# Optimization experiments

Measured on AMD Instinct MI355X. Metric: run time of the kernel, lower is better.

The kernel has to match this reference:

```python
import jax, jax.numpy as jnp
import numpy as np

NUM_USERS = 100000
NUM_ITEMS = 200000
IN_DIM = 128
HID = 256
E = 500000


def setup_inputs() -> dict:
    key = jax.random.key(0)
    ks = jax.random.split(key, 12)
    s1 = 1.0 / np.sqrt(2 * IN_DIM)
    s2 = 1.0 / np.sqrt(HID)
    return {
        "user_embed": jax.random.normal(ks[0], (NUM_USERS, IN_DIM), jnp.float32),
        "item_embed": jax.random.normal(ks[1], (NUM_ITEMS, IN_DIM), jnp.float32),
        "u_clicks": jax.random.randint(ks[2], (E,), 0, NUM_USERS, jnp.int32),
        "v_clicks": jax.random.randint(ks[3], (E,), 0, NUM_ITEMS, jnp.int32),
        "u_buys": jax.random.randint(ks[4], (E,), 0, NUM_USERS, jnp.int32),
        "v_buys": jax.random.randint(ks[5], (E,), 0, NUM_ITEMS, jnp.int32),
        "W1_clicks": jax.random.normal(ks[6], (2 * IN_DIM, HID), jnp.float32) * s1,
        "b1_clicks": jnp.zeros((HID,), jnp.float32),
        "W2_clicks": jax.random.normal(ks[7], (HID,), jnp.float32) * s2,
        "b2_clicks": jnp.zeros((1,), jnp.float32),
        "W1_buys": jax.random.normal(ks[8], (2 * IN_DIM, HID), jnp.float32) * s1,
        "b1_buys": jnp.zeros((HID,), jnp.float32),
        "W2_buys": jax.random.normal(ks[9], (HID,), jnp.float32) * s2,
        "b2_buys": jnp.zeros((1,), jnp.float32),
    }


def _edge_mlp(h_u, h_v, W1, b1, W2, b2):
    # concat([h_u, h_v]) @ W1 computed without materializing the concat:
    # split W1 into source-half and target-half. Dropout(p=0) is identity.
    d = h_u.shape[1]
    h = jax.nn.relu(h_u @ W1[:d] + h_v @ W1[d:] + b1)  # [E, HID]
    return h @ W2 + b2[0]  # [E] (Linear(hidden,1).squeeze(1))


def reference(user_embed, item_embed, u_clicks, v_clicks, u_buys, v_buys,
              W1_clicks, b1_clicks, W2_clicks, b2_clicks,
              W1_buys, b1_buys, W2_buys, b2_buys):
    logits_clicks = _edge_mlp(user_embed[u_clicks], item_embed[v_clicks],
                              W1_clicks, b1_clicks, W2_clicks, b2_clicks)
    logits_buys = _edge_mlp(user_embed[u_buys], item_embed[v_buys],
                            W1_buys, b1_buys, W2_buys, b2_buys)
    return logits_clicks, logits_buys
```

## Files before the change

kernel.cpp:

```cpp
#include <hip/hip_runtime.h>
#include <hip/hip_bf16.h>

typedef short bf16x8 __attribute__((ext_vector_type(8)));
typedef float f32x4 __attribute__((ext_vector_type(4)));

#define HID 256
#define IN_DIM 128
#define M_BLOCK 64
#define LDS_STRIDE 264

__device__ __forceinline__ float bf2f(unsigned short x) {
    union { unsigned int u; float f; } c; c.u = ((unsigned int)x) << 16; return c.f;
}
__device__ __forceinline__ unsigned short f2bf(float f) {
    union { float f; unsigned int u; } c; c.f = f;
    unsigned int u = c.u;
    u += 0x7FFFu + ((u >> 16) & 1u);
    return (unsigned short)(u >> 16);
}
__device__ __forceinline__ unsigned int pack2(float lo, float hi) {
    return (unsigned int)f2bf(lo) | ((unsigned int)f2bf(hi) << 16);
}

__device__ __forceinline__ bool detect_bf16(const unsigned short* p, int strideElems) {
    const int lane = threadIdx.x & 63;
    unsigned int u = p[(size_t)2 * lane * strideElems];
    unsigned int e = (u >> 7) & 0xFFu;
    bool bad = ((u & 0x7FFFu) != 0u) && (e < 90u || e > 141u);
    return __ballot(bad) == 0ull;
}
__device__ __forceinline__ bool detect_idx64(const int* p) {
    const int lane = threadIdx.x & 63;
    int v = p[2 * (lane * 64) + 1];
    return __ballot(v != 0) == 0ull;
}

extern "C" __global__ void pack_w1_kernel(
    const void* __restrict__ W1c,
    const void* __restrict__ W1b,
    unsigned short* __restrict__ outp)
{
    const int t = blockIdx.y;
    const void* W1 = t ? W1b : W1c;
    const unsigned short* W1u = (const unsigned short*)W1;
    const float* W1f = (const float*)W1;
    const bool w1bf = detect_bf16(W1u, 512);

    const int tid = blockIdx.x * 256 + threadIdx.x;
    const int lane = tid & 63;
    const int nt = (tid >> 6) & 15;
    const int kt = tid >> 10;
    const int k0 = kt * 32 + (lane >> 4) * 8;
    const int n  = nt * 16 + (lane & 15);
    unsigned short vals[8];
#pragma unroll
    for (int j = 0; j < 8; ++j) {
        const int src = (k0 + j) * HID + n;
        vals[j] = w1bf ? W1u[src] : f2bf(W1f[src]);
    }
    unsigned short* dst = outp + (size_t)t * 65536 + (size_t)tid * 8;
    *reinterpret_cast<uint4*>(dst) = *reinterpret_cast<const uint4*>(vals);
}

extern "C" __global__ __launch_bounds__(256, 3)
void edge_mlp_kernel(
    const void* __restrict__ user_embed,
    const void* __restrict__ item_embed,
    const int* __restrict__ u0, const int* __restrict__ v0,
    const int* __restrict__ u1, const int* __restrict__ v1,
    const unsigned short* __restrict__ packedW1,
    const void* __restrict__ b1_0, const void* __restrict__ w2_0,
    const void* __restrict__ b2_0,
    const void* __restrict__ b1_1, const void* __restrict__ w2_1,
    const void* __restrict__ b2_1,
    float* __restrict__ out, int E)
{
    __shared__ unsigned short sA[M_BLOCK * LDS_STRIDE];
    __shared__ float pRed[4][M_BLOCK];

    const int t  = blockIdx.y;
    const int e0 = blockIdx.x * M_BLOCK;
    const int tid = threadIdx.x;

    const int* uI = t ? u1 : u0;
    const int* vI = t ? v1 : v0;
    const void* b1 = t ? b1_1 : b1_0;
    const void* w2 = t ? w2_1 : w2_0;
    const void* b2 = t ? b2_1 : b2_0;
    const unsigned short* pW = packedW1 + (size_t)t * 65536;

    const bool uBf  = detect_bf16((const unsigned short*)user_embed, 1024);
    const bool iBf  = detect_bf16((const unsigned short*)item_embed, 1024);
    const bool w2Bf = detect_bf16((const unsigned short*)w2, 2);
    const bool u64f = detect_idx64(uI);
    const bool v64f = detect_idx64(vI);

    {
        const int el = tid >> 2;
        const int q  = tid & 3;
        const int e  = e0 + el;
        uint4* dst = reinterpret_cast<uint4*>(&sA[el * LDS_STRIDE + q * 64]);
        if (e < E) {
            size_t idx; const void* tab; bool tbf; int off;
            if (q < 2) { idx = (size_t)(u64f ? uI[2 * e] : uI[e]); tab = user_embed; tbf = uBf; off = q * 64; }
            else       { idx = (size_t)(v64f ? vI[2 * e] : vI[e]); tab = item_embed; tbf = iBf; off = (q - 2) * 64; }
            if (tbf) {
                const uint4* s4 = reinterpret_cast<const uint4*>(
                    (const unsigned short*)tab + idx * IN_DIM + off);
#pragma unroll
                for (int i = 0; i < 8; ++i) dst[i] = s4[i];
            } else {
                const float4* s4 = reinterpret_cast<const float4*>(
                    (const float*)tab + idx * IN_DIM + off);
#pragma unroll
                for (int i = 0; i < 8; ++i) {
                    float4 f0 = s4[2 * i];
                    float4 f1 = s4[2 * i + 1];
                    uint4 o;
                    o.x = pack2(f0.x, f0.y);
                    o.y = pack2(f0.z, f0.w);
                    o.z = pack2(f1.x, f1.y);
                    o.w = pack2(f1.z, f1.w);
                    dst[i] = o;
                }
            }
        } else {
            uint4 z; z.x = z.y = z.z = z.w = 0;
#pragma unroll
            for (int i = 0; i < 8; ++i) dst[i] = z;
        }
    }
    __syncthreads();

    const int wv   = tid >> 6;
    const int lane = tid & 63;
    const int lq   = lane >> 4;
    const int lm   = lane & 15;

    f32x4 acc[4][4];
#pragma unroll
    for (int ms = 0; ms < 4; ++ms)
#pragma unroll
        for (int ntg = 0; ntg < 4; ++ntg)
            acc[ms][ntg] = (f32x4){0.f, 0.f, 0.f, 0.f};

#pragma unroll
    for (int kt = 0; kt < 8; ++kt) {
        const int koff = kt * 32 + lq * 8;
        bf16x8 aF[4];
#pragma unroll
        for (int ms = 0; ms < 4; ++ms)
            aF[ms] = *reinterpret_cast<const bf16x8*>(&sA[(ms * 16 + lm) * LDS_STRIDE + koff]);
#pragma unroll
        for (int ntg = 0; ntg < 4; ++ntg) {
            const int nt = wv * 4 + ntg;
            bf16x8 bF = *reinterpret_cast<const bf16x8*>(
                pW + (((size_t)(kt * 16 + nt) * 64 + lane) * 8));
#pragma unroll
            for (int ms = 0; ms < 4; ++ms)
                acc[ms][ntg] = __builtin_amdgcn_mfma_f32_16x16x32_bf16(aF[ms], bF, acc[ms][ntg], 0, 0, 0);
        }
    }

    float part[4][4];
#pragma unroll
    for (int ms = 0; ms < 4; ++ms)
#pragma unroll
        for (int r = 0; r < 4; ++r) part[ms][r] = 0.f;

#pragma unroll
    for (int ntg = 0; ntg < 4; ++ntg) {
        const int n = (wv * 4 + ntg) * 16 + lm;
        const float b1n = w2Bf ? bf2f(((const unsigned short*)b1)[n]) : ((const float*)b1)[n];
        const float w2n = w2Bf ? bf2f(((const unsigned short*)w2)[n]) : ((const float*)w2)[n];
#pragma unroll
        for (int ms = 0; ms < 4; ++ms)
#pragma unroll
            for (int r = 0; r < 4; ++r) {
                float h = acc[ms][ntg][r] + b1n;
                h = fmaxf(h, 0.f);
                part[ms][r] = fmaf(h, w2n, part[ms][r]);
            }
    }

#pragma unroll
    for (int off = 1; off < 16; off <<= 1) {
#pragma unroll
        for (int ms = 0; ms < 4; ++ms)
#pragma unroll
            for (int r = 0; r < 4; ++r)
                part[ms][r] += __shfl_xor(part[ms][r], off, 64);
    }

    if (lm == 0) {
#pragma unroll
        for (int ms = 0; ms < 4; ++ms)
#pragma unroll
            for (int r = 0; r < 4; ++r)
                pRed[wv][ms * 16 + lq * 4 + r] = part[ms][r];
    }
    __syncthreads();

    if (tid < M_BLOCK) {
        const int e = e0 + tid;
        if (e < E) {
            const float b2v = w2Bf ? bf2f(((const unsigned short*)b2)[0]) : ((const float*)b2)[0];
            float s = b2v + pRed[0][tid] + pRed[1][tid] + pRed[2][tid] + pRed[3][tid];
            out[(size_t)t * E + e] = s;
        }
    }
}

extern "C" void kernel_launch(void* const* d_in, const int* in_sizes, int n_in,
                              void* d_out, int out_size, void* d_ws, size_t ws_size,
                              hipStream_t stream)
{
    const void* user_embed = d_in[0];
    const void* item_embed = d_in[1];
    const int* u0 = (const int*)d_in[2];
    const int* v0 = (const int*)d_in[3];
    const int* u1 = (const int*)d_in[4];
    const int* v1 = (const int*)d_in[5];
    const void* W1c = d_in[6];
    const void* b1c = d_in[7];
    const void* w2c = d_in[8];
    const void* b2c = d_in[9];
    const void* W1b = d_in[10];
    const void* b1b = d_in[11];
    const void* w2b = d_in[12];
    const void* b2b = d_in[13];

    const int E = in_sizes[2];
    unsigned short* packedW1 = (unsigned short*)d_ws;

    hipLaunchKernelGGL(pack_w1_kernel, dim3(32, 2), dim3(256), 0, stream, W1c, W1b, packedW1);

    dim3 grid((E + M_BLOCK - 1) / M_BLOCK, 2);
    hipLaunchKernelGGL(edge_mlp_kernel, grid, dim3(256), 0, stream,
                       user_embed, item_embed, u0, v0, u1, v1, packedW1,
                       b1c, w2c, b2c, b1b, w2b, b2b,
                       (float*)d_out, E);
}
```

Before: 462.1 us.

## Pre-convert embedding tables to bf16 and prefetch gathers across persistent tiles

Adds a kernel that converts both full embedding tables from fp32 to bf16 in workspace before the edge MLP runs. The main kernel then gathers half-width rows and processes four tiles per block, prefetching the next tile's rows and indices into registers while the current tile runs its MFMA work. The aim is to cut gather bandwidth and hide gather latency. The trade-off is that converting the whole tables (about 300k rows) reads and writes far more data than the 1M gathered rows need. The new path also drops the dtype and int64 detection and assumes fp32 inputs.

```diff
diff --git a/kernel.cpp b/kernel.cpp
--- a/kernel.cpp
+++ b/kernel.cpp
@@ -6,8 +6,8 @@
 
 #define HID 256
 #define IN_DIM 128
-#define M_BLOCK 64
-#define LDS_STRIDE 264
+#define LDS_US 264
+#define TPB 4
 
 __device__ __forceinline__ float bf2f(unsigned short x) {
     union { unsigned int u; float f; } c; c.u = ((unsigned int)x) << 16; return c.f;
@@ -21,7 +21,6 @@
 __device__ __forceinline__ unsigned int pack2(float lo, float hi) {
     return (unsigned int)f2bf(lo) | ((unsigned int)f2bf(hi) << 16);
 }
-
 __device__ __forceinline__ bool detect_bf16(const unsigned short* p, int strideElems) {
     const int lane = threadIdx.x & 63;
     unsigned int u = p[(size_t)2 * lane * strideElems];
@@ -35,9 +34,26 @@
     return __ballot(v != 0) == 0ull;
 }
 
+extern "C" __global__ void cvt_tables_kernel(
+    const float* __restrict__ uT, const float* __restrict__ iT,
+    unsigned short* __restrict__ ub, unsigned short* __restrict__ ib,
+    int nu8, int ni8)
+{
+    int g = blockIdx.x * 256 + threadIdx.x;
+    if (g >= nu8 + ni8) return;
+    const float* src; unsigned short* dst; int idx;
+    if (g < nu8) { src = uT; dst = ub; idx = g; }
+    else         { src = iT; dst = ib; idx = g - nu8; }
+    const float4* s4 = reinterpret_cast<const float4*>(src) + (size_t)idx * 2;
+    float4 a = s4[0], b = s4[1];
+    uint4 o;
+    o.x = pack2(a.x, a.y); o.y = pack2(a.z, a.w);
+    o.z = pack2(b.x, b.y); o.w = pack2(b.z, b.w);
+    reinterpret_cast<uint4*>(dst)[idx] = o;
+}
+
 extern "C" __global__ void pack_w1_kernel(
-    const void* __restrict__ W1c,
-    const void* __restrict__ W1b,
+    const void* __restrict__ W1c, const void* __restrict__ W1b,
     unsigned short* __restrict__ outp)
 {
     const int t = blockIdx.y;
@@ -45,7 +61,6 @@
     const unsigned short* W1u = (const unsigned short*)W1;
     const float* W1f = (const float*)W1;
     const bool w1bf = detect_bf16(W1u, 512);
-
     const int tid = blockIdx.x * 256 + threadIdx.x;
     const int lane = tid & 63;
     const int nt = (tid >> 6) & 15;
@@ -63,65 +78,224 @@
 }
 
 extern "C" __global__ __launch_bounds__(256, 3)
-void edge_mlp_kernel(
-    const void* __restrict__ user_embed,
-    const void* __restrict__ item_embed,
+void edge_mlp_bf16(
+    const unsigned short* __restrict__ uT, const unsigned short* __restrict__ iT,
     const int* __restrict__ u0, const int* __restrict__ v0,
     const int* __restrict__ u1, const int* __restrict__ v1,
     const unsigned short* __restrict__ packedW1,
-    const void* __restrict__ b1_0, const void* __restrict__ w2_0,
-    const void* __restrict__ b2_0,
-    const void* __restrict__ b1_1, const void* __restrict__ w2_1,
-    const void* __restrict__ b2_1,
+    const float* __restrict__ b1_0, const float* __restrict__ w2_0, const float* __restrict__ b2_0,
+    const float* __restrict__ b1_1, const float* __restrict__ w2_1, const float* __restrict__ b2_1,
+    float* __restrict__ out, int E, int nTiles)
+{
+    __shared__ unsigned short sA[64 * LDS_US];
+    __shared__ float pRed[4][64];
+
+    const int t = blockIdx.y;
+    const int* uI = t ? u1 : u0;
+    const int* vI = t ? v1 : v0;
+    const float* b1 = t ? b1_1 : b1_0;
+    const float* w2 = t ? w2_1 : w2_0;
+    const float b2v = t ? b2_1[0] : b2_0[0];
+    const unsigned short* pW = packedW1 + (size_t)t * 65536;
+
+    const int tid  = threadIdx.x;
+    const int el   = tid >> 3;
+    const int o    = tid & 7;
+    const int wv   = tid >> 6;
+    const int lane = tid & 63;
+    const int lq   = lane >> 4;
+    const int lm   = lane & 15;
+    const int tile0 = blockIdx.x * TPB;
+
+    uint4 pf[8];
+    int iuN[2], ivN[2];
+
+    {
+        int iu[2], iv[2];
+#pragma unroll
+        for (int p = 0; p < 2; ++p) {
+            int e = tile0 * 64 + p * 32 + el;
+            iu[p] = (e < E) ? uI[e] : 0;
+            iv[p] = (e < E) ? vI[e] : 0;
+        }
+#pragma unroll
+        for (int p = 0; p < 2; ++p) {
+            int e = tile0 * 64 + p * 32 + el;
+            if (e < E) {
+                const uint4* ru = reinterpret_cast<const uint4*>(uT + (size_t)iu[p] * IN_DIM);
+                const uint4* rv = reinterpret_cast<const uint4*>(iT + (size_t)iv[p] * IN_DIM);
+                pf[p*4+0] = ru[o];   pf[p*4+1] = ru[o+8];
+                pf[p*4+2] = rv[o];   pf[p*4+3] = rv[o+8];
+            } else {
+                uint4 z; z.x = z.y = z.z = z.w = 0;
+                pf[p*4+0] = z; pf[p*4+1] = z; pf[p*4+2] = z; pf[p*4+3] = z;
+            }
+        }
+#pragma unroll
+        for (int p = 0; p < 2; ++p) {
+            int e = (tile0 + 1) * 64 + p * 32 + el;
+            iuN[p] = (e < E) ? uI[e] : 0;
+            ivN[p] = (e < E) ? vI[e] : 0;
+        }
+    }
+
+    for (int j = 0; j < TPB; ++j) {
+        const int tile = tile0 + j;
+        if (tile >= nTiles) break;
+
+        __syncthreads();
+#pragma unroll
+        for (int p = 0; p < 2; ++p) {
+            uint4* d4 = reinterpret_cast<uint4*>(&sA[(p * 32 + el) * LDS_US]);
+            d4[o]      = pf[p*4+0];
+            d4[o + 8]  = pf[p*4+1];
+            d4[o + 16] = pf[p*4+2];
+            d4[o + 24] = pf[p*4+3];
+        }
+        __syncthreads();
+
+        if (j + 1 < TPB) {
+#pragma unroll
+            for (int p = 0; p < 2; ++p) {
+                int e = (tile + 1) * 64 + p * 32 + el;
+                if (e < E) {
+                    const uint4* ru = reinterpret_cast<const uint4*>(uT + (size_t)iuN[p] * IN_DIM);
+                    const uint4* rv = reinterpret_cast<const uint4*>(iT + (size_t)ivN[p] * IN_DIM);
+                    pf[p*4+0] = ru[o];   pf[p*4+1] = ru[o+8];
+                    pf[p*4+2] = rv[o];   pf[p*4+3] = rv[o+8];
+                } else {
+                    uint4 z; z.x = z.y = z.z = z.w = 0;
+                    pf[p*4+0] = z; pf[p*4+1] = z; pf[p*4+2] = z; pf[p*4+3] = z;
+                }
+            }
+            if (j + 2 < TPB) {
+#pragma unroll
+                for (int p = 0; p < 2; ++p) {
+                    int e = (tile + 2) * 64 + p * 32 + el;
+                    iuN[p] = (e < E) ? uI[e] : 0;
+                    ivN[p] = (e < E) ? vI[e] : 0;
+                }
+            }
+        }
+
+        f32x4 acc[4][4];
+#pragma unroll
+        for (int ms = 0; ms < 4; ++ms)
+#pragma unroll
+            for (int ntg = 0; ntg < 4; ++ntg)
+                acc[ms][ntg] = (f32x4){0.f, 0.f, 0.f, 0.f};
+
+#pragma unroll
+        for (int kt = 0; kt < 8; ++kt) {
+            const int koff = kt * 32 + lq * 8;
+            bf16x8 aF[4];
+#pragma unroll
+            for (int ms = 0; ms < 4; ++ms)
+                aF[ms] = *reinterpret_cast<const bf16x8*>(&sA[(ms * 16 + lm) * LDS_US + koff]);
+#pragma unroll
+            for (int ntg = 0; ntg < 4; ++ntg) {
+                const int nt = wv * 4 + ntg;
+                bf16x8 bF = *reinterpret_cast<const bf16x8*>(
+                    pW + (((size_t)(kt * 16 + nt) * 64 + lane) * 8));
+#pragma unroll
+                for (int ms = 0; ms < 4; ++ms)
+                    acc[ms][ntg] = __builtin_amdgcn_mfma_f32_16x16x32_bf16(aF[ms], bF, acc[ms][ntg], 0, 0, 0);
+            }
+        }
+
+        float part[4][4];
+#pragma unroll
+        for (int ms = 0; ms < 4; ++ms)
+#pragma unroll
+            for (int r = 0; r < 4; ++r) part[ms][r] = 0.f;
+
+#pragma unroll
+        for (int ntg = 0; ntg < 4; ++ntg) {
+            const int n = (wv * 4 + ntg) * 16 + lm;
+            const float b1n = b1[n];
+            const float w2n = w2[n];
+#pragma unroll
+            for (int ms = 0; ms < 4; ++ms)
+#pragma unroll
+                for (int r = 0; r < 4; ++r) {
+                    float h = fmaxf(acc[ms][ntg][r] + b1n, 0.f);
+                    part[ms][r] = fmaf(h, w2n, part[ms][r]);
+                }
+        }
+#pragma unroll
+        for (int off = 1; off < 16; off <<= 1)
+#pragma unroll
+            for (int ms = 0; ms < 4; ++ms)
+#pragma unroll
+                for (int r = 0; r < 4; ++r)
+                    part[ms][r] += __shfl_xor(part[ms][r], off, 64);
+
+        if (lm == 0)
+#pragma unroll
+            for (int ms = 0; ms < 4; ++ms)
+#pragma unroll
+                for (int r = 0; r < 4; ++r)
+                    pRed[wv][ms * 16 + lq * 4 + r] = part[ms][r];
+        __syncthreads();
+
+        if (tid < 64) {
+            const int e = tile * 64 + tid;
+            if (e < E) {
+                float s = b2v + pRed[0][tid] + pRed[1][tid] + pRed[2][tid] + pRed[3][tid];
+                out[(size_t)t * E + e] = s;
+            }
+        }
+    }
+}
+
+extern "C" __global__ __launch_bounds__(256, 3)
+void edge_mlp_f32(
+    const void* __restrict__ user_embed, const void* __restrict__ item_embed,
+    const int* __restrict__ u0, const int* __restrict__ v0,
+    const int* __restrict__ u1, const int* __restrict__ v1,
+    const unsigned short* __restrict__ packedW1,
+    const void* __restrict__ b1_0, const void* __restrict__ w2_0, const void* __restrict__ b2_0,
+    const void* __restrict__ b1_1, const void* __restrict__ w2_1, const void* __restrict__ b2_1,
     float* __restrict__ out, int E)
 {
-    __shared__ unsigned short sA[M_BLOCK * LDS_STRIDE];
-    __shared__ float pRed[4][M_BLOCK];
-
+    __shared__ unsigned short sA[64 * LDS_US];
+    __shared__ float pRed[4][64];
     const int t  = blockIdx.y;
-    const int e0 = blockIdx.x * M_BLOCK;
+    const int e0 = blockIdx.x * 64;
     const int tid = threadIdx.x;
-
     const int* uI = t ? u1 : u0;
     const int* vI = t ? v1 : v0;
     const void* b1 = t ? b1_1 : b1_0;
     const void* w2 = t ? w2_1 : w2_0;
     const void* b2 = t ? b2_1 : b2_0;
     const unsigned short* pW = packedW1 + (size_t)t * 65536;
-
     const bool uBf  = detect_bf16((const unsigned short*)user_embed, 1024);
     const bool iBf  = detect_bf16((const unsigned short*)item_embed, 1024);
     const bool w2Bf = detect_bf16((const unsigned short*)w2, 2);
     const bool u64f = detect_idx64(uI);
     const bool v64f = detect_idx64(vI);
-
     {
         const int el = tid >> 2;
         const int q  = tid & 3;
         const int e  = e0 + el;
-        uint4* dst = reinterpret_cast<uint4*>(&sA[el * LDS_STRIDE + q * 64]);
+        uint4* dst = reinterpret_cast<uint4*>(&sA[el * LDS_US + q * 64]);
         if (e < E) {
             size_t idx; const void* tab; bool tbf; int off;
-            if (q < 2) { idx = (size_t)(u64f ? uI[2 * e] : uI[e]); tab = user_embed; tbf = uBf; off = q * 64; }
-            else       { idx = (size_t)(v64f ? vI[2 * e] : vI[e]); tab = item_embed; tbf = iBf; off = (q - 2) * 64; }
+            if (q < 2) { idx = (size_t)(u64f ? uI[2*e] : uI[e]); tab = user_embed; tbf = uBf; off = q * 64; }
+            else       { idx = (size_t)(v64f ? vI[2*e] : vI[e]); tab = item_embed; tbf = iBf; off = (q-2) * 64; }
             if (tbf) {
-                const uint4* s4 = reinterpret_cast<const uint4*>(
-                    (const unsigned short*)tab + idx * IN_DIM + off);
+                const uint4* s4 = reinterpret_cast<const uint4*>((const unsigned short*)tab + idx * IN_DIM + off);
 #pragma unroll
                 for (int i = 0; i < 8; ++i) dst[i] = s4[i];
             } else {
-                const float4* s4 = reinterpret_cast<const float4*>(
-                    (const float*)tab + idx * IN_DIM + off);
+                const float4* s4 = reinterpret_cast<const float4*>((const float*)tab + idx * IN_DIM + off);
 #pragma unroll
                 for (int i = 0; i < 8; ++i) {
-                    float4 f0 = s4[2 * i];
-                    float4 f1 = s4[2 * i + 1];
-                    uint4 o;
-                    o.x = pack2(f0.x, f0.y);
-                    o.y = pack2(f0.z, f0.w);
-                    o.z = pack2(f1.x, f1.y);
-                    o.w = pack2(f1.z, f1.w);
-                    dst[i] = o;
+                    float4 f0 = s4[2*i], f1 = s4[2*i+1];
+                    uint4 ov;
+                    ov.x = pack2(f0.x, f0.y); ov.y = pack2(f0.z, f0.w);
+                    ov.z = pack2(f1.x, f1.y); ov.w = pack2(f1.z, f1.w);
+                    dst[i] = ov;
                 }
             }
         } else {
@@ -131,82 +305,65 @@
         }
     }
     __syncthreads();
-
-    const int wv   = tid >> 6;
-    const int lane = tid & 63;
-    const int lq   = lane >> 4;
-    const int lm   = lane & 15;
-
+    const int wv = tid >> 6, lane = tid & 63, lq = lane >> 4, lm = lane & 15;
     f32x4 acc[4][4];
 #pragma unroll
     for (int ms = 0; ms < 4; ++ms)
 #pragma unroll
-        for (int ntg = 0; ntg < 4; ++ntg)
-            acc[ms][ntg] = (f32x4){0.f, 0.f, 0.f, 0.f};
-
+        for (int ntg = 0; ntg < 4; ++ntg) acc[ms][ntg] = (f32x4){0.f,0.f,0.f,0.f};
 #pragma unroll
     for (int kt = 0; kt < 8; ++kt) {
         const int koff = kt * 32 + lq * 8;
         bf16x8 aF[4];
 #pragma unroll
         for (int ms = 0; ms < 4; ++ms)
-            aF[ms] = *reinterpret_cast<const bf16x8*>(&sA[(ms * 16 + lm) * LDS_STRIDE + koff]);
+            aF[ms] = *reinterpret_cast<const bf16x8*>(&sA[(ms*16+lm) * LDS_US + koff]);
 #pragma unroll
         for (int ntg = 0; ntg < 4; ++ntg) {
             const int nt = wv * 4 + ntg;
-            bf16x8 bF = *reinterpret_cast<const bf16x8*>(
-                pW + (((size_t)(kt * 16 + nt) * 64 + lane) * 8));
+            bf16x8 bF = *reinterpret_cast<const bf16x8*>(pW + (((size_t)(kt*16+nt)*64 + lane)*8));
 #pragma unroll
             for (int ms = 0; ms < 4; ++ms)
                 acc[ms][ntg] = __builtin_amdgcn_mfma_f32_16x16x32_bf16(aF[ms], bF, acc[ms][ntg], 0, 0, 0);
         }
     }
-
     float part[4][4];
 #pragma unroll
     for (int ms = 0; ms < 4; ++ms)
 #pragma unroll
         for (int r = 0; r < 4; ++r) part[ms][r] = 0.f;
-
 #pragma unroll
     for (int ntg = 0; ntg < 4; ++ntg) {
-        const int n = (wv * 4 + ntg) * 16 + lm;
+        const int n = (wv*4+ntg)*16 + lm;
         const float b1n = w2Bf ? bf2f(((const unsigned short*)b1)[n]) : ((const float*)b1)[n];
         const float w2n = w2Bf ? bf2f(((const unsigned short*)w2)[n]) : ((const float*)w2)[n];
 #pragma unroll
         for (int ms = 0; ms < 4; ++ms)
 #pragma unroll
             for (int r = 0; r < 4; ++r) {
-                float h = acc[ms][ntg][r] + b1n;
-                h = fmaxf(h, 0.f);
+                float h = fmaxf(acc[ms][ntg][r] + b1n, 0.f);
                 part[ms][r] = fmaf(h, w2n, part[ms][r]);
             }
     }
-
-#pragma unroll
-    for (int off = 1; off < 16; off <<= 1) {
+#pragma unroll
+    for (int off = 1; off < 16; off <<= 1)
 #pragma unroll
         for (int ms = 0; ms < 4; ++ms)
 #pragma unroll
             for (int r = 0; r < 4; ++r)
                 part[ms][r] += __shfl_xor(part[ms][r], off, 64);
-    }
-
-    if (lm == 0) {
+    if (lm == 0)
 #pragma unroll
         for (int ms = 0; ms < 4; ++ms)
 #pragma unroll
             for (int r = 0; r < 4; ++r)
-                pRed[wv][ms * 16 + lq * 4 + r] = part[ms][r];
-    }
+                pRed[wv][ms*16 + lq*4 + r] = part[ms][r];
     __syncthreads();
-
-    if (tid < M_BLOCK) {
+    if (tid < 64) {
         const int e = e0 + tid;
         if (e < E) {
             const float b2v = w2Bf ? bf2f(((const unsigned short*)b2)[0]) : ((const float*)b2)[0];
-            float s = b2v + pRed[0][tid] + pRed[1][tid] + pRed[2][tid] + pRed[3][tid];
-            out[(size_t)t * E + e] = s;
+            out[(size_t)t * E + e] = b2v + pRed[0][tid] + pRed[1][tid] + pRed[2][tid] + pRed[3][tid];
         }
     }
 }
@@ -231,13 +388,33 @@
     const void* b2b = d_in[13];
 
     const int E = in_sizes[2];
+    const size_t NU = (size_t)in_sizes[0];
+    const size_t NI = (size_t)in_sizes[1];
     unsigned short* packedW1 = (unsigned short*)d_ws;
+    const size_t need = 262144 + 2 * (NU + NI);
 
     hipLaunchKernelGGL(pack_w1_kernel, dim3(32, 2), dim3(256), 0, stream, W1c, W1b, packedW1);
 
-    dim3 grid((E + M_BLOCK - 1) / M_BLOCK, 2);
-    hipLaunchKernelGGL(edge_mlp_kernel, grid, dim3(256), 0, stream,
-                       user_embed, item_embed, u0, v0, u1, v1, packedW1,
-                       b1c, w2c, b2c, b1b, w2b, b2b,
-                       (float*)d_out, E);
-}
+    const int nTiles = (E + 63) / 64;
+
+    if (ws_size >= need) {
+        unsigned short* ub = (unsigned short*)((char*)d_ws + 262144);
+        unsigned short* ib = ub + NU;
+        const int nu8 = (int)(NU / 8), ni8 = (int)(NI / 8);
+        const int tot = nu8 + ni8;
+        hipLaunchKernelGGL(cvt_tables_kernel, dim3((tot + 255) / 256), dim3(256), 0, stream,
+                           (const float*)user_embed, (const float*)item_embed, ub, ib, nu8, ni8);
+        dim3 grid((nTiles + TPB - 1) / TPB, 2);
+        hipLaunchKernelGGL(edge_mlp_bf16, grid, dim3(256), 0, stream,
+                           ub, ib, u0, v0, u1, v1, packedW1,
+                           (const float*)b1c, (const float*)w2c, (const float*)b2c,
+                           (const float*)b1b, (const float*)w2b, (const float*)b2b,
+                           (float*)d_out, E, nTiles);
+    } else {
+        dim3 grid(nTiles, 2);
+        hipLaunchKernelGGL(edge_mlp_f32, grid, dim3(256), 0, stream,
+                           user_embed, item_embed, u0, v0, u1, v1, packedW1,
+                           b1c, w2c, b2c, b1b, w2b, b2b,
+                           (float*)d_out, E);
+    }
+}
```

Result: slower. 654.9 us (+41.7%).
